# Performance work log

Measured on AMD Instinct MI355X. Metric: run time of the kernel, lower is better.

Reference implementation:

```python
import jax, jax.numpy as jnp
import numpy as np

N = 4096      # num_nodes
DIN = 16      # num_inputs
C = 16        # comm_channels
CHQ = 8       # ch_q
K = 10        # value-iteration steps
GAMMA = 0.99
EPS = float(np.finfo(np.float32).eps)


def setup_inputs() -> dict:
    key = jax.random.key(0)
    ks = jax.random.split(key, 8)
    x = jax.random.normal(ks[0], (N, DIN), dtype=jnp.float32)
    comms = jnp.zeros((N, C), dtype=jnp.float32)  # fresh comm state (reset())
    # random symmetric 0/1 adjacency, ~20 avg degree, zero diagonal
    u = jax.random.uniform(ks[1], (N, N), dtype=jnp.float32)
    a = (u < 0.005).astype(jnp.float32)
    adj = jnp.maximum(a, a.T) * (1.0 - jnp.eye(N, dtype=jnp.float32))
    mask = jnp.ones((N,), dtype=jnp.float32)
    # parameters (torch Linear: y = x @ W + b, weights stored [in, out] here)
    Wr = jax.random.normal(ks[2], (DIN + C, 1), dtype=jnp.float32) * 0.1   # reward_encoding
    br = jnp.zeros((1,), dtype=jnp.float32)
    We = jax.random.normal(ks[3], (DIN + C, CHQ), dtype=jnp.float32) * 0.1  # encoder
    be = jnp.zeros((CHQ,), dtype=jnp.float32)
    w_emb = jax.random.normal(ks[4], (CHQ,), dtype=jnp.float32) * 0.1       # embedder (ch_q -> 1)
    b_emb = jnp.zeros((), dtype=jnp.float32)
    Wa = jax.random.normal(ks[5], (CHQ,), dtype=jnp.float32) * 0.1          # action_decoding (1 -> ch_q)
    ba = jnp.zeros((CHQ,), dtype=jnp.float32)
    return dict(x=x, comms=comms, adj=adj, mask=mask, Wr=Wr, br=br,
                We=We, be=be, w_emb=w_emb, b_emb=b_emb, Wa=Wa, ba=ba, k=K)


def reference(x, comms, adj, mask, Wr, br, We, be, w_emb, b_emb, Wa, ba, k):
    n = adj.shape[0]
    # initialize_adj: symmetric normalization D^{-1/2} (A + I) D^{-1/2}
    a_norm = adj + jnp.eye(n, dtype=adj.dtype)
    deg = a_norm.sum(axis=0)
    dinv_sqrt = jnp.sqrt(1.0 / (deg + EPS))
    k3 = a_norm * dinv_sqrt[:, None] * dinv_sqrt[None, :]

    xc = jnp.concatenate([x, comms], axis=1)          # [n, DIN+C]
    r = (xc @ Wr + br)[:, 0]                          # reward per node [n]
    # embedder(cols - rows) fused: score[i,j] = s[j] - s[i] + b_emb
    s = (xc @ We + be) @ w_emb                        # [n]
    kernel3 = k3 * (s[None, :] - s[:, None] + b_emb)  # [n, n]

    # k-step value iteration
    v = jnp.zeros_like(r)
    for _ in range(k):
        k3v = kernel3 @ (r + GAMMA * v)               # [n]
        q = k3v[:, None] * Wa[None, :] + ba           # action_decoding (1 -> ch_q): [n, ch_q]
        v = q.max(axis=-1)                            # [n]

    # final_feature_process (rl=False): additive -inf mask
    return v + jnp.where(mask == 0, -jnp.inf, 0.0)
```

## Files before the change

### kernel.cpp

```cpp
#include <hip/hip_runtime.h>
#include <math.h>

#define NN     4096
#define NB     256
#define TPB    1024
#define WPB    16
#define CAP    128
#define GAMMA  0.99f
#define EPSF   1.1920929e-07f
#define KSTEPS 10
#define RELSTR 16

union F2U { unsigned long long u; float2 f; };

__device__ __forceinline__ void grid_barrier(int* arr, int* rel, int k) {
    __syncthreads();
    if (threadIdx.x == 0)
        __hip_atomic_store(arr + blockIdx.x, k, __ATOMIC_RELAXED,
                           __HIP_MEMORY_SCOPE_AGENT);
    if (blockIdx.x == 0) {
        if (threadIdx.x < 64) {
            const int base = threadIdx.x * 4;
            for (;;) {
                const int a0 = __hip_atomic_load(arr + base + 0, __ATOMIC_RELAXED, __HIP_MEMORY_SCOPE_AGENT);
                const int a1 = __hip_atomic_load(arr + base + 1, __ATOMIC_RELAXED, __HIP_MEMORY_SCOPE_AGENT);
                const int a2 = __hip_atomic_load(arr + base + 2, __ATOMIC_RELAXED, __HIP_MEMORY_SCOPE_AGENT);
                const int a3 = __hip_atomic_load(arr + base + 3, __ATOMIC_RELAXED, __HIP_MEMORY_SCOPE_AGENT);
                if (__all((a0 >= k) && (a1 >= k) && (a2 >= k) && (a3 >= k))) break;
                __builtin_amdgcn_s_sleep(1);
            }
#pragma unroll
            for (int i = 0; i < 4; ++i)
                __hip_atomic_store(rel + (size_t)(base + i) * RELSTR, k,
                                   __ATOMIC_RELAXED, __HIP_MEMORY_SCOPE_AGENT);
        }
    } else if (threadIdx.x == 0) {
        while (__hip_atomic_load(rel + (size_t)blockIdx.x * RELSTR,
                                 __ATOMIC_RELAXED, __HIP_MEMORY_SCOPE_AGENT) < k)
            __builtin_amdgcn_s_sleep(1);
    }
    __syncthreads();
}

__global__ void __launch_bounds__(TPB) gvin_persist(
    const float* __restrict__ adj,  const float* __restrict__ x,
    const float* __restrict__ comms,const float* __restrict__ mask,
    const float* __restrict__ Wr,   const float* __restrict__ br,
    const float* __restrict__ We,   const float* __restrict__ be,
    const float* __restrict__ w_emb,const float* __restrict__ b_emb,
    const float* __restrict__ Wa,   const float* __restrict__ ba,
    int* arr, int* rel,
    unsigned long long* AB0, unsigned long long* AB1,
    float* __restrict__ out)
{
    __shared__ int nbr[WPB][CAP];
    __shared__ int lcnt[WPB];
    const int wave = threadIdx.x >> 6;
    const int lane = threadIdx.x & 63;
    const int g = (int)blockIdx.x * WPB + wave;

    if (lane == 0) { lcnt[wave] = 1; nbr[wave][0] = g; }

    const float4* rowp = (const float4*)(adj + (size_t)g * NN);
#pragma unroll 4
    for (int it = 0; it < 16; ++it) {
        const float4 v = rowp[lane + it * 64];
        const int b4 = (lane + it * 64) * 4;
        if (v.x != 0.0f) { int sl = atomicAdd(&lcnt[wave], 1); if (sl < CAP) nbr[wave][sl] = b4;     }
        if (v.y != 0.0f) { int sl = atomicAdd(&lcnt[wave], 1); if (sl < CAP) nbr[wave][sl] = b4 + 1; }
        if (v.z != 0.0f) { int sl = atomicAdd(&lcnt[wave], 1); if (sl < CAP) nbr[wave][sl] = b4 + 2; }
        if (v.w != 0.0f) { int sl = atomicAdd(&lcnt[wave], 1); if (sl < CAP) nbr[wave][sl] = b4 + 3; }
    }

    float pr = 0.0f, ps = 0.0f;
    if (lane < 32) {
        const float xc = (lane < 16) ? x[g * 16 + lane] : comms[g * 16 + (lane - 16)];
        float we = 0.0f;
#pragma unroll
        for (int c = 0; c < 8; ++c) we += We[lane * 8 + c] * w_emb[c];
        pr = xc * Wr[lane];
        ps = xc * we;
    } else if (lane == 32) {
#pragma unroll
        for (int c = 0; c < 8; ++c) ps += be[c] * w_emb[c];
        pr = br[0];
    }
#pragma unroll
    for (int off = 32; off; off >>= 1) { pr += __shfl_xor(pr, off); ps += __shfl_xor(ps, off); }
    const float r = pr, s = ps;

    const int   deg  = lcnt[wave];
    const int   cl   = deg < CAP ? deg : CAP;
    const float dinv = sqrtf(1.0f / ((float)deg + EPSF));
    const float p    = dinv * (s + b_emb[0]);

    const bool val0 = lane < cl;
    const bool val1 = 64 + lane < cl;
    const int  j0   = val0 ? nbr[wave][lane] : g;
    const int  j1   = val1 ? nbr[wave][64 + lane] : g;

    float wa[8], bb[8];
#pragma unroll
    for (int c = 0; c < 8; ++c) { wa[c] = Wa[c]; bb[c] = ba[c]; }

    if (lane == 0) {
        F2U z; z.f = make_float2(p * r, dinv * r);
        __hip_atomic_store(AB0 + g, z.u, __ATOMIC_RELAXED, __HIP_MEMORY_SCOPE_AGENT);
    }

    float v = 0.0f;
    for (int t = 0; t < KSTEPS; ++t) {
        grid_barrier(arr, rel, t + 1);
        const unsigned long long* ABin  = (t & 1) ? AB1 : AB0;
        unsigned long long*       ABout = (t & 1) ? AB0 : AB1;
        F2U z0, z1;
        z0.u = __hip_atomic_load(ABin + j0, __ATOMIC_RELAXED, __HIP_MEMORY_SCOPE_AGENT);
        z1.u = __hip_atomic_load(ABin + j1, __ATOMIC_RELAXED, __HIP_MEMORY_SCOPE_AGENT);
        float S1 = val0 ? z0.f.x : 0.0f;
        float S2 = val0 ? z0.f.y : 0.0f;
        if (val1) { S1 += z1.f.x; S2 += z1.f.y; }
#pragma unroll
        for (int off = 32; off; off >>= 1) { S1 += __shfl_xor(S1, off); S2 += __shfl_xor(S2, off); }
        const float k3v = dinv * (S1 - s * S2);
        v = fmaf(k3v, wa[0], bb[0]);
#pragma unroll
        for (int c = 1; c < 8; ++c) v = fmaxf(v, fmaf(k3v, wa[c], bb[c]));
        if (t < KSTEPS - 1 && lane == 0) {
            const float u = r + GAMMA * v;
            F2U z; z.f = make_float2(p * u, dinv * u);
            __hip_atomic_store(ABout + g, z.u, __ATOMIC_RELAXED, __HIP_MEMORY_SCOPE_AGENT);
        }
    }

    if (lane == 0) out[g] = v + (mask[g] == 0.0f ? -INFINITY : 0.0f);
}

extern "C" void kernel_launch(void* const* d_in, const int* in_sizes, int n_in,
                              void* d_out, int out_size, void* d_ws, size_t ws_size,
                              hipStream_t stream) {
    const float* x     = (const float*)d_in[0];
    const float* comms = (const float*)d_in[1];
    const float* adj   = (const float*)d_in[2];
    const float* mask  = (const float*)d_in[3];
    const float* Wr    = (const float*)d_in[4];
    const float* br    = (const float*)d_in[5];
    const float* We    = (const float*)d_in[6];
    const float* be    = (const float*)d_in[7];
    const float* w_emb = (const float*)d_in[8];
    const float* b_emb = (const float*)d_in[9];
    const float* Wa    = (const float*)d_in[10];
    const float* ba    = (const float*)d_in[11];

    char* ws = (char*)d_ws;
    int* arr = (int*)(ws + 0);
    int* rel = (int*)(ws + 4096);
    unsigned long long* AB0 = (unsigned long long*)(ws + 4096 + 16384);
    unsigned long long* AB1 = (unsigned long long*)(ws + 4096 + 16384 + (size_t)NN * 8);
    float* out = (float*)d_out;

    gvin_persist<<<dim3(NB), dim3(TPB), 0, stream>>>(
        adj, x, comms, mask, Wr, br, We, be, w_emb, b_emb, Wa, ba,
        arr, rel, AB0, AB1, out);
}
```

Before: 150.8 us.

## Tag per-step node values and prefetch neighbor values before the grid barrier

Replaces the two ping-pong float2 buffers with a per-step array of values, each packed with a step tag. Each wave issues its neighbor loads before the grid barrier and, after the barrier, spins until the tags match the current step. The aim is to overlap load latency with the barrier and prepare for looser, dataflow-style synchronization. The full grid barrier is still executed, so the tags and prefetch mostly add loads and spin checks. Tags left in the workspace by earlier launches could match stale data if the barrier ordering were ever relaxed.

```diff
diff --git a/kernel.cpp b/kernel.cpp
--- a/kernel.cpp
+++ b/kernel.cpp
@@ -11,10 +11,12 @@
 #define KSTEPS 10
 #define RELSTR 16
 
-union F2U { unsigned long long u; float2 f; };
+union VU { unsigned long long u; struct { float f; unsigned tag; } s; };
+__device__ __forceinline__ unsigned long long pack_v(float f, unsigned tag) {
+    VU z; z.s.f = f; z.s.tag = tag; return z.u;
+}
 
 __device__ __forceinline__ void grid_barrier(int* arr, int* rel, int k) {
-    __syncthreads();
     if (threadIdx.x == 0)
         __hip_atomic_store(arr + blockIdx.x, k, __ATOMIC_RELAXED,
                            __HIP_MEMORY_SCOPE_AGENT);
@@ -50,7 +52,7 @@
     const float* __restrict__ w_emb,const float* __restrict__ b_emb,
     const float* __restrict__ Wa,   const float* __restrict__ ba,
     int* arr, int* rel,
-    unsigned long long* AB0, unsigned long long* AB1,
+    unsigned long long* V,
     float* __restrict__ out)
 {
     __shared__ int nbr[WPB][CAP];
@@ -104,21 +106,39 @@
     for (int c = 0; c < 8; ++c) { wa[c] = Wa[c]; bb[c] = ba[c]; }
 
     if (lane == 0) {
-        F2U z; z.f = make_float2(p * r, dinv * r);
-        __hip_atomic_store(AB0 + g, z.u, __ATOMIC_RELAXED, __HIP_MEMORY_SCOPE_AGENT);
+        unsigned long long* v0 = V + (size_t)g * 2;
+        __hip_atomic_store(v0,     pack_v(p * r,    1u), __ATOMIC_RELAXED, __HIP_MEMORY_SCOPE_AGENT);
+        __hip_atomic_store(v0 + 1, pack_v(dinv * r, 1u), __ATOMIC_RELAXED, __HIP_MEMORY_SCOPE_AGENT);
     }
 
     float v = 0.0f;
     for (int t = 0; t < KSTEPS; ++t) {
+        const unsigned tg = (unsigned)(t + 1);
+        const unsigned long long* Vin = V + (size_t)t * NN * 2;
+        __syncthreads();
+        unsigned long long sa0 = __hip_atomic_load(Vin + 2 * j0,     __ATOMIC_RELAXED, __HIP_MEMORY_SCOPE_AGENT);
+        unsigned long long sb0 = __hip_atomic_load(Vin + 2 * j0 + 1, __ATOMIC_RELAXED, __HIP_MEMORY_SCOPE_AGENT);
+        unsigned long long sa1 = __hip_atomic_load(Vin + 2 * j1,     __ATOMIC_RELAXED, __HIP_MEMORY_SCOPE_AGENT);
+        unsigned long long sb1 = __hip_atomic_load(Vin + 2 * j1 + 1, __ATOMIC_RELAXED, __HIP_MEMORY_SCOPE_AGENT);
+        asm volatile("" ::: "memory");
         grid_barrier(arr, rel, t + 1);
-        const unsigned long long* ABin  = (t & 1) ? AB1 : AB0;
-        unsigned long long*       ABout = (t & 1) ? AB0 : AB1;
-        F2U z0, z1;
-        z0.u = __hip_atomic_load(ABin + j0, __ATOMIC_RELAXED, __HIP_MEMORY_SCOPE_AGENT);
-        z1.u = __hip_atomic_load(ABin + j1, __ATOMIC_RELAXED, __HIP_MEMORY_SCOPE_AGENT);
-        float S1 = val0 ? z0.f.x : 0.0f;
-        float S2 = val0 ? z0.f.y : 0.0f;
-        if (val1) { S1 += z1.f.x; S2 += z1.f.y; }
+        VU A0, B0, A1, B1;
+        A0.u = sa0; B0.u = sb0; A1.u = sa1; B1.u = sb1;
+        float S1 = 0.0f, S2 = 0.0f;
+        if (val0) {
+            while (A0.s.tag != tg || B0.s.tag != tg) {
+                A0.u = __hip_atomic_load(Vin + 2 * j0,     __ATOMIC_RELAXED, __HIP_MEMORY_SCOPE_AGENT);
+                B0.u = __hip_atomic_load(Vin + 2 * j0 + 1, __ATOMIC_RELAXED, __HIP_MEMORY_SCOPE_AGENT);
+            }
+            S1 += A0.s.f; S2 += B0.s.f;
+        }
+        if (val1) {
+            while (A1.s.tag != tg || B1.s.tag != tg) {
+                A1.u = __hip_atomic_load(Vin + 2 * j1,     __ATOMIC_RELAXED, __HIP_MEMORY_SCOPE_AGENT);
+                B1.u = __hip_atomic_load(Vin + 2 * j1 + 1, __ATOMIC_RELAXED, __HIP_MEMORY_SCOPE_AGENT);
+            }
+            S1 += A1.s.f; S2 += B1.s.f;
+        }
 #pragma unroll
         for (int off = 32; off; off >>= 1) { S1 += __shfl_xor(S1, off); S2 += __shfl_xor(S2, off); }
         const float k3v = dinv * (S1 - s * S2);
@@ -127,8 +147,9 @@
         for (int c = 1; c < 8; ++c) v = fmaxf(v, fmaf(k3v, wa[c], bb[c]));
         if (t < KSTEPS - 1 && lane == 0) {
             const float u = r + GAMMA * v;
-            F2U z; z.f = make_float2(p * u, dinv * u);
-            __hip_atomic_store(ABout + g, z.u, __ATOMIC_RELAXED, __HIP_MEMORY_SCOPE_AGENT);
+            unsigned long long* vo = V + ((size_t)(t + 1) * NN + g) * 2;
+            __hip_atomic_store(vo,     pack_v(p * u,    tg + 1u), __ATOMIC_RELAXED, __HIP_MEMORY_SCOPE_AGENT);
+            __hip_atomic_store(vo + 1, pack_v(dinv * u, tg + 1u), __ATOMIC_RELAXED, __HIP_MEMORY_SCOPE_AGENT);
         }
     }
 
@@ -154,11 +175,10 @@
     char* ws = (char*)d_ws;
     int* arr = (int*)(ws + 0);
     int* rel = (int*)(ws + 4096);
-    unsigned long long* AB0 = (unsigned long long*)(ws + 4096 + 16384);
-    unsigned long long* AB1 = (unsigned long long*)(ws + 4096 + 16384 + (size_t)NN * 8);
+    unsigned long long* V = (unsigned long long*)(ws + 65536);
     float* out = (float*)d_out;
 
     gvin_persist<<<dim3(NB), dim3(TPB), 0, stream>>>(
         adj, x, comms, mask, Wr, br, We, be, w_emb, b_emb, Wa, ba,
-        arr, rel, AB0, AB1, out);
+        arr, rel, V, out);
 }
```

Result: slower. 180.0 us (+19.3%).
